# Performance work log

Measured on AMD Instinct MI355X. Metric: run time of the kernel, lower is better.

The kernel has to match this reference:

```python
import jax, jax.numpy as jnp
import numpy as np

B, N = 4096, 12
HID = 64
SLOPE = 0.2   # GATv2Conv default negative_slope
ALPHA = 0.1   # skip-connection scale


def _gabriel_adjacency(p):
    # p: [B, N, 2] node positions. Gabriel graph: edge (i,j) iff no other
    # point k lies inside the closed disk with diameter segment (p_i, p_j).
    n = p.shape[1]
    mid = (p[:, :, None, :] + p[:, None, :, :]) * 0.5                      # [B,N,N,2]
    r2 = jnp.sum((p[:, :, None, :] - p[:, None, :, :]) ** 2, -1) * 0.25    # [B,N,N]
    d2 = jnp.sum((p[:, None, None, :, :] - mid[:, :, :, None, :]) ** 2, -1)  # [B,i,j,k]
    eye = jnp.eye(n, dtype=bool)
    excl = eye[:, None, :] | eye[None, :, :]                               # k==i or k==j
    d2 = jnp.where(excl[None], jnp.inf, d2)
    gab = jnp.all(d2 > r2[..., None], axis=-1) & (~eye)[None]
    # undirected edges + self loops (GATv2Conv add_self_loops=True default)
    return gab | jnp.swapaxes(gab, 1, 2) | eye[None]                       # [B,N,N]


def _gatv2(x, adj, wl, wr, att, b):
    # PyG GATv2Conv, heads=1: e_ij = att . leaky_relu(W_l x_j + W_r x_i),
    # alpha = softmax_j(e_ij) over neighbors, out_i = sum_j alpha_ij W_l x_j + b.
    xl = x @ wl                                                            # source feats [B,N,H]
    xr = x @ wr                                                            # target feats [B,N,H]
    s = jax.nn.leaky_relu(xl[:, None, :, :] + xr[:, :, None, :], SLOPE)    # [B,i,j,H]
    e = jnp.einsum('bijh,h->bij', s, att)
    e = jnp.where(adj, e, -1e9)
    a = jax.nn.softmax(e, axis=-1)                                         # over sources j
    return jnp.einsum('bij,bjh->bih', a, xl) + b


def _forward(batch, enc_w1, enc_b1, enc_w2, enc_b2, enc_w3, enc_b3,
             g1_wl, g1_wr, g1_att, g1_b, g2_wl, g2_wr, g2_att, g2_b,
             g3_wl, g3_wr, g3_att, g3_b, g4_wl, g4_wr, g4_att, g4_b,
             lab_w, lab_b, val_w, val_b, skip_w, skip_b):
    h = jax.nn.relu(batch @ enc_w1 + enc_b1)
    h = jax.nn.relu(h @ enc_w2 + enc_b2)
    latent = h @ enc_w3 + enc_b3                                           # [B,N,3]
    # graph construction is non-differentiable (scipy in the original)
    adj = _gabriel_adjacency(jax.lax.stop_gradient(latent[..., :2]))
    x0 = latent[..., 2:3]                                                  # [B,N,1]
    x1 = jax.nn.relu(_gatv2(x0, adj, g1_wl, g1_wr, g1_att, g1_b))
    x2 = jax.nn.relu(_gatv2(x1, adj, g2_wl, g2_wr, g2_att, g2_b))
    skip = latent @ skip_w + skip_b
    x3 = jax.nn.relu(_gatv2(x2, adj, g3_wl, g3_wr, g3_att, g3_b) + ALPHA * skip)
    logits = x3 @ lab_w + lab_b                                            # [B,N,4]
    # note: original feeds x2 (not x3) into gcn4 -- kept faithful
    x4 = jax.nn.relu(_gatv2(x2, adj, g4_wl, g4_wr, g4_att, g4_b) + ALPHA * skip)
    values = x4 @ val_w + val_b                                            # [B,N,1]
    return batch[:, :, :4], batch[:, :, 4:5], logits, values, latent


def setup_inputs():
    key = jax.random.key(0)
    ks = iter(jax.random.split(key, 40))
    def rnd(shape, s=0.1):
        return jax.random.normal(next(ks), shape, dtype=jnp.float32) * s
    inp = {"batch": jax.random.normal(next(ks), (B, N, 5), dtype=jnp.float32)}
    inp.update(enc_w1=rnd((5, HID)), enc_b1=jnp.zeros((HID,), jnp.float32),
               enc_w2=rnd((HID, HID)), enc_b2=jnp.zeros((HID,), jnp.float32),
               enc_w3=rnd((HID, 3)), enc_b3=jnp.zeros((3,), jnp.float32))
    for i, cin in zip((1, 2, 3, 4), (1, HID, HID, HID)):
        inp[f"g{i}_wl"] = rnd((cin, HID)); inp[f"g{i}_wr"] = rnd((cin, HID))
        inp[f"g{i}_att"] = rnd((HID,)); inp[f"g{i}_b"] = jnp.zeros((HID,), jnp.float32)
    inp.update(lab_w=rnd((HID, 4)), lab_b=jnp.zeros((4,), jnp.float32),
               val_w=rnd((HID, 1)), val_b=jnp.zeros((1,), jnp.float32),
               skip_w=rnd((3, HID)), skip_b=jnp.zeros((HID,), jnp.float32))
    return inp


def reference(batch, enc_w1, enc_b1, enc_w2, enc_b2, enc_w3, enc_b3,
              g1_wl, g1_wr, g1_att, g1_b, g2_wl, g2_wr, g2_att, g2_b,
              g3_wl, g3_wr, g3_att, g3_b, g4_wl, g4_wr, g4_att, g4_b,
              lab_w, lab_b, val_w, val_b, skip_w, skip_b):
    return _forward(batch, enc_w1, enc_b1, enc_w2, enc_b2, enc_w3, enc_b3,
                    g1_wl, g1_wr, g1_att, g1_b, g2_wl, g2_wr, g2_att, g2_b,
                    g3_wl, g3_wr, g3_att, g3_b, g4_wl, g4_wr, g4_att, g4_b,
                    lab_w, lab_b, val_w, val_b, skip_w, skip_b)
```

## Files before the change

kernel.cpp:

```cpp
#include <hip/hip_runtime.h>
#include <hip/hip_bf16.h>
#include <math.h>

#define N     12
#define HID   64
#define STP   68
#define SLOPE 0.2f
#define ALPHA 0.1f

typedef float v2f __attribute__((ext_vector_type(2)));
typedef float v4f __attribute__((ext_vector_type(4)));
typedef int   i4  __attribute__((ext_vector_type(4)));
typedef short v8s __attribute__((ext_vector_type(8)));

static __device__ __forceinline__ v8s as_v8s(i4 v) {
    union { i4 a; v8s b; } u; u.a = v; return u.b;
}

#define OUT0 0
#define OUT1 196608
#define OUT2 245760
#define OUT3 442368
#define OUT4 491520

__global__ void prep_kernel(const float* __restrict__ enc_w2,
                            const float* __restrict__ g2_wl, const float* __restrict__ g2_wr,
                            const float* __restrict__ g3_wl, const float* __restrict__ g3_wr,
                            const float* __restrict__ g4_wl, const float* __restrict__ g4_wr,
                            const float* __restrict__ lab_w,
                            float* __restrict__ ws) {
    int t = threadIdx.x;
    int bx = blockIdx.x;
    if (bx < 64) {
        int c = bx;
        ws[t*64 + c] = enc_w2[c*64 + t];
        return;
    }
    if (bx == 112) {
        #pragma unroll
        for (int c = 0; c < 4; c++) ws[16384 + c*64 + t] = lab_w[t*4 + c];
        return;
    }
    int idx = bx - 64;
    int mat = idx >> 3, rem = idx & 7;
    int kt = rem >> 2, nt = rem & 3;
    const float* src;
    switch (mat) {
        case 0: src = g2_wl; break;
        case 1: src = g2_wr; break;
        case 2: src = g3_wl; break;
        case 3: src = g3_wr; break;
        case 4: src = g4_wl; break;
        default: src = g4_wr; break;
    }
    int quad = t >> 4, col = t & 15;
    int n = nt*16 + col;
    unsigned* dst = (unsigned*)(ws + 4096) + mat*2048 + (kt*4+nt)*256 + t*4;
    #pragma unroll
    for (int jp = 0; jp < 4; jp++) {
        int k0 = kt*32 + quad*8 + 2*jp;
        __hip_bfloat16 h0 = __float2bfloat16(src[(k0+0)*64 + n]);
        __hip_bfloat16 h1 = __float2bfloat16(src[(k0+1)*64 + n]);
        unsigned u0 = *(unsigned short*)&h0, u1 = *(unsigned short*)&h1;
        dst[jp] = u0 | (u1 << 16);
    }
}

template<bool TW>
__global__ __launch_bounds__(64, 3) void gae_kernel(
    const float* __restrict__ batch,
    const float* __restrict__ enc_w1, const float* __restrict__ enc_b1,
    const float* __restrict__ enc_w2, const float* __restrict__ enc_b2,
    const float* __restrict__ enc_w3, const float* __restrict__ enc_b3,
    const float* __restrict__ g1_wl, const float* __restrict__ g1_wr,
    const float* __restrict__ g1_att, const float* __restrict__ g1_b,
    const float* __restrict__ g2_wl, const float* __restrict__ g2_wr,
    const float* __restrict__ g2_att, const float* __restrict__ g2_b,
    const float* __restrict__ g3_wl, const float* __restrict__ g3_wr,
    const float* __restrict__ g3_att, const float* __restrict__ g3_b,
    const float* __restrict__ g4_wl, const float* __restrict__ g4_wr,
    const float* __restrict__ g4_att, const float* __restrict__ g4_b,
    const float* __restrict__ lab_w, const float* __restrict__ lab_b,
    const float* __restrict__ val_w, const float* __restrict__ val_b,
    const float* __restrict__ skip_w, const float* __restrict__ skip_b,
    const float* __restrict__ wsT,
    float* __restrict__ out)
{
    const int b = blockIdx.x;
    const int t = threadIdx.x;

    __shared__ __align__(16) float lds[2560];
    float* bufL = lds;
    float* bufR = lds + N*STP;
    float* xB   = lds + 2*N*STP;
    float* pool = lds + 2*N*STP + N*HID;
    unsigned char* pairs8 = (unsigned char*)&lds[2544];

    const v2f z2 = {0.f, 0.f};
    const v4f z4 = {0.f, 0.f, 0.f, 0.f};
    const v4f s4 = {SLOPE, SLOPE, SLOPE, SLOPE};

    const int p0 = t,        i0 = p0 / N, j0 = p0 - i0*N;
    const int p1 = t + 64,   i1 = p1 / N, j1 = p1 - i1*N;
    const int p2 = (t < 16) ? (t + 128) : 143;
    const int i2 = p2 / N,   j2 = p2 - i2*N;

    if (t < N*5) {
        float v = batch[b*(N*5) + t];
        pool[t] = v;
        int i = t / 5, f = t - i*5;
        if (f < 4) out[OUT0 + (size_t)b*(N*4) + i*4 + f] = v;
        else       out[OUT1 + (size_t)b*N + i] = v;
    }
    __syncthreads();

    {
        float acc[N];
        float bias = enc_b1[t];
        #pragma unroll
        for (int i=0;i<N;i++) acc[i] = bias;
        #pragma unroll
        for (int f=0; f<5; f++) {
            float w = enc_w1[f*HID + t];
            #pragma unroll
            for (int i=0;i<N;i++) acc[i] = fmaf(pool[i*5+f], w, acc[i]);
        }
        #pragma unroll
        for (int i=0;i<N;i++) bufL[i*STP + t] = fmaxf(acc[i], 0.f);
    }
    __syncthreads();

    {
        v2f acc[N];
        #pragma unroll
        for (int i=0;i<N;i++) acc[i] = z2;
        const float* w2p = TW ? (wsT + t*HID) : nullptr;
        for (int c=0;c<HID;c+=4) {
            v2f w01, w23;
            if (TW) {
                v4f w4 = *reinterpret_cast<const v4f*>(&w2p[c]);
                w01 = w4.xy; w23 = w4.zw;
            } else {
                w01 = (v2f){enc_w2[(c+0)*HID+t], enc_w2[(c+1)*HID+t]};
                w23 = (v2f){enc_w2[(c+2)*HID+t], enc_w2[(c+3)*HID+t]};
            }
            #pragma unroll
            for (int i=0;i<N;i++) {
                v4f xv = *reinterpret_cast<const v4f*>(&bufL[i*STP + c]);
                acc[i] = __builtin_elementwise_fma(xv.xy, w01, acc[i]);
                acc[i] = __builtin_elementwise_fma(xv.zw, w23, acc[i]);
            }
        }
        float bias = enc_b2[t];
        #pragma unroll
        for (int i=0;i<N;i++) bufR[i*STP + t] = fmaxf(bias + acc[i].x + acc[i].y, 0.f);
    }
    __syncthreads();

    if (t < N*3) {
        int i = t / 3, c = t - i*3;
        float acc = enc_b3[c];
        for (int k=0;k<HID;k+=4) {
            v4f xv = *reinterpret_cast<const v4f*>(&bufR[i*STP + k]);
            acc = fmaf(xv.x, enc_w3[(k+0)*3+c], acc);
            acc = fmaf(xv.y, enc_w3[(k+1)*3+c], acc);
            acc = fmaf(xv.z, enc_w3[(k+2)*3+c], acc);
            acc = fmaf(xv.w, enc_w3[(k+3)*3+c], acc);
        }
        pool[t] = acc;
        out[OUT4 + (size_t)b*(N*3) + t] = acc;
    }
    __syncthreads();

    float skipv[N];
    {
        float w0 = skip_w[t], w1 = skip_w[HID+t], w2 = skip_w[2*HID+t];
        float bias = skip_b[t];
        #pragma unroll
        for (int i=0;i<N;i++) {
            float v = bias;
            v = fmaf(pool[i*3+0], w0, v);
            v = fmaf(pool[i*3+1], w1, v);
            v = fmaf(pool[i*3+2], w2, v);
            skipv[i] = v;
        }
    }

    auto gab = [&](int i, int j)->bool {
        if (i == j) return false;
        float pix = pool[i*3], piy = pool[i*3+1];
        float pjx = pool[j*3], pjy = pool[j*3+1];
        float mx = (pix + pjx) * 0.5f, my = (piy + pjy) * 0.5f;
        float dx = pix - pjx, dy = piy - pjy;
        float r2 = (dx*dx + dy*dy) * 0.25f;
        bool g = true;
        #pragma unroll
        for (int k=0;k<N;k++) {
            float ex = pool[k*3] - mx, ey = pool[k*3+1] - my;
            bool ok = (k == i) || (k == j) || (ex*ex + ey*ey > r2);
            g = g && ok;
        }
        return g;
    };
    unsigned long long gb0 = __ballot(gab(i0, j0));
    unsigned long long gb1 = __ballot(gab(i1, j1));
    unsigned long long gb2 = __ballot((t < 16) && gab(i2, j2));
    auto gbit = [&](int p)->int {
        unsigned long long m = (p < 64) ? gb0 : ((p < 128) ? gb1 : gb2);
        return (int)((m >> (p & 63)) & 1ull);
    };
    const int adjA = gbit(p0) | gbit(j0*N+i0) | (i0 == j0);
    const int adjB = gbit(p1) | gbit(j1*N+i1) | (i1 == j1);
    const int adjC = (t < 16) ? (gbit(p2) | gbit(j2*N+i2) | (i2 == j2)) : 0;

    auto mbcnt64 = [&](unsigned long long m)->int {
        return __builtin_amdgcn_mbcnt_hi((unsigned)(m >> 32),
               __builtin_amdgcn_mbcnt_lo((unsigned)m, 0));
    };
    const unsigned long long am0 = __ballot(adjA != 0);
    const unsigned long long am1 = __ballot(adjB != 0);
    const unsigned long long am2 = __ballot(adjC != 0);
    const int c0  = __popcll(am0);
    const int c01 = c0 + __popcll(am1);
    const int nv  = c01 + __popcll(am2);
    const int idx0 = mbcnt64(am0);
    const int idx1 = c0  + mbcnt64(am1);
    const int idx2 = c01 + mbcnt64(am2);
    if (adjA)               pairs8[idx0] = (unsigned char)p0;
    if (adjB && idx1 < 64)  pairs8[idx1] = (unsigned char)p1;
    if (adjC && idx2 < 64)  pairs8[idx2] = (unsigned char)p2;
    const bool ovB = adjB && (idx1 >= 64);
    const bool ovC = adjC && (idx2 >= 64);
    const int nvc = nv < 64 ? nv : 64;

    auto scoreAt = [&](int i, int j, const float* __restrict__ att)->float {
        const float* Lj = &bufL[j*STP];
        const float* Ri = &bufR[i*STP];
        v4f a = z4;
        for (int h=0; h<HID; h+=4) {
            v4f a4 = *reinterpret_cast<const v4f*>(&att[h]);
            v4f xl = *reinterpret_cast<const v4f*>(Lj + h);
            v4f xr = *reinterpret_cast<const v4f*>(Ri + h);
            v4f s = xl + xr;
            v4f l = __builtin_elementwise_fma(s4, __builtin_elementwise_min(s, z4),
                                              __builtin_elementwise_max(s, z4));
            a = __builtin_elementwise_fma(a4, l, a);
        }
        return (a.x + a.y) + (a.z + a.w);
    };

    auto gat_core = [&](const float* __restrict__ att, const float* __restrict__ gb,
                        float* __restrict__ xout, int strideOut, int useSkip) {
        __syncthreads();
        pool[t] = -1e9f; pool[t+64] = -1e9f;
        if (t < 16) pool[t+128] = -1e9f;
        if (t < nvc) {
            int p = pairs8[t];
            int i = (p * 171) >> 11;
            int j = p - i*N;
            pool[p] = scoreAt(i, j, att);
        }
        if (nv > 64) {
            if (ovB) pool[p1] = scoreAt(i1, j1, att);
            if (ovC) pool[p2] = scoreAt(i2, j2, att);
        }
        __syncthreads();
        if (t < N) {
            float m = -2e9f;
            #pragma unroll
            for (int j=0;j<N;j++) m = fmaxf(m, pool[t*N+j]);
            float tmp[N]; float sum = 0.f;
            #pragma unroll
            for (int j=0;j<N;j++) { float v = __expf(pool[t*N+j] - m); tmp[j] = v; sum += v; }
            float inv = 1.0f / sum;
            #pragma unroll
            for (int j=0;j<N;j++) pool[t*N+j] = tmp[j] * inv;
        }
        __syncthreads();
        {
            float xj[N];
            #pragma unroll
            for (int j=0;j<N;j++) xj[j] = bufL[j*STP + t];
            v4f X0 = {xj[0], xj[1], xj[2],  xj[3]};
            v4f X1 = {xj[4], xj[5], xj[6],  xj[7]};
            v4f X2 = {xj[8], xj[9], xj[10], xj[11]};
            float bias = gb[t];
            #pragma unroll
            for (int i=0;i<N;i++) {
                const v4f* ep = reinterpret_cast<const v4f*>(&pool[i*N]);
                v4f acc = __builtin_elementwise_fma(ep[0], X0,
                          __builtin_elementwise_fma(ep[1], X1, ep[2]*X2));
                float r = bias + ((acc.x + acc.y) + (acc.z + acc.w));
                if (useSkip) r = fmaf(ALPHA, skipv[i], r);
                xout[i*strideOut + t] = fmaxf(r, 0.f);
            }
        }
        __syncthreads();
    };

    auto stage_mfma = [&](const float* __restrict__ xin, int strideIn, int matL) {
        const int m = t & 15, quad = t >> 4;
        const int mc = (m < N) ? m : 0;
        i4 aF[2];
        #pragma unroll
        for (int kt=0; kt<2; kt++) {
            const float* xp = &xin[mc*strideIn + kt*32 + quad*8];
            v4f lo = *reinterpret_cast<const v4f*>(xp);
            v4f hi = *reinterpret_cast<const v4f*>(xp + 4);
            unsigned u0 = __float_as_uint(lo.x) + 0x8000u, u1 = __float_as_uint(lo.y) + 0x8000u;
            unsigned u2 = __float_as_uint(lo.z) + 0x8000u, u3 = __float_as_uint(lo.w) + 0x8000u;
            unsigned u4 = __float_as_uint(hi.x) + 0x8000u, u5 = __float_as_uint(hi.y) + 0x8000u;
            unsigned u6 = __float_as_uint(hi.z) + 0x8000u, u7 = __float_as_uint(hi.w) + 0x8000u;
            i4 a;
            a.x = (int)__builtin_amdgcn_perm(u1, u0, 0x07060302u);
            a.y = (int)__builtin_amdgcn_perm(u3, u2, 0x07060302u);
            a.z = (int)__builtin_amdgcn_perm(u5, u4, 0x07060302u);
            a.w = (int)__builtin_amdgcn_perm(u7, u6, 0x07060302u);
            aF[kt] = a;
        }
        const i4* bbase = reinterpret_cast<const i4*>(wsT + 4096);
        #pragma unroll
        for (int mm=0; mm<2; mm++) {
            const i4* bp = bbase + (matL + mm)*512;
            v4f acc[4] = {z4, z4, z4, z4};
            #pragma unroll
            for (int nt=0; nt<4; nt++) {
                i4 b0 = bp[(0*4+nt)*64 + t];
                i4 b1 = bp[(1*4+nt)*64 + t];
                acc[nt] = __builtin_amdgcn_mfma_f32_16x16x32_bf16(as_v8s(aF[0]), as_v8s(b0), acc[nt], 0, 0, 0);
                acc[nt] = __builtin_amdgcn_mfma_f32_16x16x32_bf16(as_v8s(aF[1]), as_v8s(b1), acc[nt], 0, 0, 0);
            }
            float* dst = (mm == 0) ? bufL : bufR;
            if (quad < 3) {
                #pragma unroll
                for (int nt=0; nt<4; nt++) {
                    #pragma unroll
                    for (int r=0; r<4; r++)
                        dst[(quad*4+r)*STP + nt*16 + m] = acc[nt][r];
                }
            }
        }
    };

    auto stage = [&](const float* __restrict__ xin, int strideIn,
                     const float* __restrict__ wl, const float* __restrict__ wr) {
        v2f al[N], ar[N];
        #pragma unroll
        for (int i=0;i<N;i++) { al[i] = z2; ar[i] = z2; }
        for (int c=0;c<HID;c+=4) {
            v2f wl01 = (v2f){wl[(c+0)*HID+t], wl[(c+1)*HID+t]};
            v2f wl23 = (v2f){wl[(c+2)*HID+t], wl[(c+3)*HID+t]};
            v2f wr01 = (v2f){wr[(c+0)*HID+t], wr[(c+1)*HID+t]};
            v2f wr23 = (v2f){wr[(c+2)*HID+t], wr[(c+3)*HID+t]};
            #pragma unroll
            for (int i=0;i<N;i++) {
                v4f xv = *reinterpret_cast<const v4f*>(&xin[i*strideIn + c]);
                al[i] = __builtin_elementwise_fma(xv.xy, wl01, al[i]);
                al[i] = __builtin_elementwise_fma(xv.zw, wl23, al[i]);
                ar[i] = __builtin_elementwise_fma(xv.xy, wr01, ar[i]);
                ar[i] = __builtin_elementwise_fma(xv.zw, wr23, ar[i]);
            }
        }
        #pragma unroll
        for (int i=0;i<N;i++) {
            bufL[i*STP + t] = al[i].x + al[i].y;
            bufR[i*STP + t] = ar[i].x + ar[i].y;
        }
    };

    {
        float wlv = g1_wl[t], wrv = g1_wr[t];
        #pragma unroll
        for (int i=0;i<N;i++) {
            float v = pool[i*3+2];
            bufL[i*STP + t] = v * wlv;
            bufR[i*STP + t] = v * wrv;
        }
    }
    gat_core(g1_att, g1_b, bufR, STP, 0);

    if (TW) stage_mfma(bufR, STP, 0); else stage(bufR, STP, g2_wl, g2_wr);
    gat_core(g2_att, g2_b, xB, HID, 0);

    if (TW) stage_mfma(xB, HID, 2); else stage(xB, HID, g3_wl, g3_wr);
    gat_core(g3_att, g3_b, bufR, STP, 1);

    if (t < N*4) {
        int i = t >> 2, c = t & 3;
        float acc = lab_b[c];
        if (TW) {
            const float* lwT = wsT + 16384 + c*HID;
            for (int h=0;h<HID;h+=4) {
                v4f xv = *reinterpret_cast<const v4f*>(&bufR[i*STP + h]);
                v4f w4 = *reinterpret_cast<const v4f*>(&lwT[h]);
                acc = fmaf(xv.x, w4.x, acc);
                acc = fmaf(xv.y, w4.y, acc);
                acc = fmaf(xv.z, w4.z, acc);
                acc = fmaf(xv.w, w4.w, acc);
            }
        } else {
            for (int h=0;h<HID;h+=4) {
                v4f xv = *reinterpret_cast<const v4f*>(&bufR[i*STP + h]);
                acc = fmaf(xv.x, lab_w[(h+0)*4+c], acc);
                acc = fmaf(xv.y, lab_w[(h+1)*4+c], acc);
                acc = fmaf(xv.z, lab_w[(h+2)*4+c], acc);
                acc = fmaf(xv.w, lab_w[(h+3)*4+c], acc);
            }
        }
        out[OUT2 + (size_t)b*(N*4) + t] = acc;
    }

    if (TW) stage_mfma(xB, HID, 4); else stage(xB, HID, g4_wl, g4_wr);
    gat_core(g4_att, g4_b, bufR, STP, 1);

    if (t < N) {
        float acc = val_b[0];
        for (int h=0;h<HID;h+=4) {
            v4f xv = *reinterpret_cast<const v4f*>(&bufR[t*STP + h]);
            v4f w4 = *reinterpret_cast<const v4f*>(&val_w[h]);
            acc = fmaf(xv.x, w4.x, acc);
            acc = fmaf(xv.y, w4.y, acc);
            acc = fmaf(xv.z, w4.z, acc);
            acc = fmaf(xv.w, w4.w, acc);
        }
        out[OUT3 + (size_t)b*N + t] = acc;
    }
}

extern "C" void kernel_launch(void* const* d_in, const int* in_sizes, int n_in,
                              void* d_out, int out_size, void* d_ws, size_t ws_size,
                              hipStream_t stream) {
    (void)in_sizes; (void)n_in; (void)out_size;
    const bool useT = (ws_size >= (16384 + 256)*sizeof(float));
    if (useT) {
        prep_kernel<<<dim3(113), dim3(64), 0, stream>>>(
            (const float*)d_in[3],
            (const float*)d_in[11], (const float*)d_in[12],
            (const float*)d_in[15], (const float*)d_in[16],
            (const float*)d_in[19], (const float*)d_in[20],
            (const float*)d_in[23],
            (float*)d_ws);
        gae_kernel<true><<<dim3(4096), dim3(64), 0, stream>>>(
            (const float*)d_in[0],
            (const float*)d_in[1],  (const float*)d_in[2],
            (const float*)d_in[3],  (const float*)d_in[4],
            (const float*)d_in[5],  (const float*)d_in[6],
            (const float*)d_in[7],  (const float*)d_in[8],  (const float*)d_in[9],  (const float*)d_in[10],
            (const float*)d_in[11], (const float*)d_in[12], (const float*)d_in[13], (const float*)d_in[14],
            (const float*)d_in[15], (const float*)d_in[16], (const float*)d_in[17], (const float*)d_in[18],
            (const float*)d_in[19], (const float*)d_in[20], (const float*)d_in[21], (const float*)d_in[22],
            (const float*)d_in[23], (const float*)d_in[24],
            (const float*)d_in[25], (const float*)d_in[26],
            (const float*)d_in[27], (const float*)d_in[28],
            (const float*)d_ws,
            (float*)d_out);
    } else {
        gae_kernel<false><<<dim3(4096), dim3(64), 0, stream>>>(
            (const float*)d_in[0],
            (const float*)d_in[1],  (const float*)d_in[2],
            (const float*)d_in[3],  (const float*)d_in[4],
            (const float*)d_in[5],  (const float*)d_in[6],
            (const float*)d_in[7],  (const float*)d_in[8],  (const float*)d_in[9],  (const float*)d_in[10],
            (const float*)d_in[11], (const float*)d_in[12], (const float*)d_in[13], (const float*)d_in[14],
            (const float*)d_in[15], (const float*)d_in[16], (const float*)d_in[17], (const float*)d_in[18],
            (const float*)d_in[19], (const float*)d_in[20], (const float*)d_in[21], (const float*)d_in[22],
            (const float*)d_in[23], (const float*)d_in[24],
            (const float*)d_in[25], (const float*)d_in[26],
            (const float*)d_in[27], (const float*)d_in[28],
            nullptr,
            (float*)d_out);
    }
}
```

Before: 155.1 us.

## Split each graph across two wavefronts with row-partitioned work and per-wave MFMA matrices

Launches 128 threads per graph instead of 64. Each wavefront owns six of the twelve node rows for the encoder, softmax and aggregation, and the two waves split the left and right projection matrices in the MFMA stage. Score computation is halved across lane groups and recombined with shuffles, and the Gabriel adjacency ballots are exchanged through LDS. The aim is more parallel work per graph and lower per-thread register pressure, enabling higher occupancy. The cost is extra barriers and cross-wave LDS traffic.

New measurement: 207.4 us. 33.7% more time.

```diff
diff --git a/kernel.cpp b/kernel.cpp
--- a/kernel.cpp
+++ b/kernel.cpp
@@ -67,7 +67,7 @@
 }
 
 template<bool TW>
-__global__ __launch_bounds__(64, 3) void gae_kernel(
+__global__ __launch_bounds__(128, 8) void gae_kernel(
     const float* __restrict__ batch,
     const float* __restrict__ enc_w1, const float* __restrict__ enc_b1,
     const float* __restrict__ enc_w2, const float* __restrict__ enc_b2,
@@ -88,218 +88,283 @@
 {
     const int b = blockIdx.x;
     const int t = threadIdx.x;
-
-    __shared__ __align__(16) float lds[2560];
-    float* bufL = lds;
-    float* bufR = lds + N*STP;
-    float* xB   = lds + 2*N*STP;
-    float* pool = lds + 2*N*STP + N*HID;
-    unsigned char* pairs8 = (unsigned char*)&lds[2544];
+    const int w = t >> 6;
+    const int l = t & 63;
+    const int r0 = w * 6;
+
+    __shared__ __align__(16) float lds[2544];
+    float* bufL  = lds;
+    float* bufR  = lds + N*STP;
+    float* xB    = lds + 2*N*STP;
+    float* pool  = lds + 2*N*STP + N*HID;
+    float* coord = pool + 108;
 
     const v2f z2 = {0.f, 0.f};
     const v4f z4 = {0.f, 0.f, 0.f, 0.f};
     const v4f s4 = {SLOPE, SLOPE, SLOPE, SLOPE};
 
-    const int p0 = t,        i0 = p0 / N, j0 = p0 - i0*N;
-    const int p1 = t + 64,   i1 = p1 / N, j1 = p1 - i1*N;
-    const int p2 = (t < 16) ? (t + 128) : 143;
-    const int i2 = p2 / N,   j2 = p2 - i2*N;
-
-    if (t < N*5) {
-        float v = batch[b*(N*5) + t];
-        pool[t] = v;
-        int i = t / 5, f = t - i*5;
+    if (l < 30) {
+        int idx = w*30 + l;
+        float v = batch[b*(N*5) + idx];
+        pool[idx] = v;
+        int i = idx / 5, f = idx - (idx/5)*5;
         if (f < 4) out[OUT0 + (size_t)b*(N*4) + i*4 + f] = v;
         else       out[OUT1 + (size_t)b*N + i] = v;
     }
-    __syncthreads();
 
     {
-        float acc[N];
-        float bias = enc_b1[t];
-        #pragma unroll
-        for (int i=0;i<N;i++) acc[i] = bias;
+        float acc[6];
+        float bias = enc_b1[l];
+        #pragma unroll
+        for (int i=0;i<6;i++) acc[i] = bias;
         #pragma unroll
         for (int f=0; f<5; f++) {
-            float w = enc_w1[f*HID + t];
-            #pragma unroll
-            for (int i=0;i<N;i++) acc[i] = fmaf(pool[i*5+f], w, acc[i]);
-        }
-        #pragma unroll
-        for (int i=0;i<N;i++) bufL[i*STP + t] = fmaxf(acc[i], 0.f);
-    }
-    __syncthreads();
+            float wv = enc_w1[f*HID + l];
+            #pragma unroll
+            for (int i=0;i<6;i++) acc[i] = fmaf(pool[(r0+i)*5+f], wv, acc[i]);
+        }
+        #pragma unroll
+        for (int i=0;i<6;i++) bufL[(r0+i)*STP + l] = fmaxf(acc[i], 0.f);
+    }
 
     {
-        v2f acc[N];
-        #pragma unroll
-        for (int i=0;i<N;i++) acc[i] = z2;
-        const float* w2p = TW ? (wsT + t*HID) : nullptr;
+        v2f acc[6];
+        #pragma unroll
+        for (int i=0;i<6;i++) acc[i] = z2;
+        const float* w2p = TW ? (wsT + l*HID) : nullptr;
         for (int c=0;c<HID;c+=4) {
             v2f w01, w23;
             if (TW) {
                 v4f w4 = *reinterpret_cast<const v4f*>(&w2p[c]);
                 w01 = w4.xy; w23 = w4.zw;
             } else {
-                w01 = (v2f){enc_w2[(c+0)*HID+t], enc_w2[(c+1)*HID+t]};
-                w23 = (v2f){enc_w2[(c+2)*HID+t], enc_w2[(c+3)*HID+t]};
-            }
-            #pragma unroll
-            for (int i=0;i<N;i++) {
-                v4f xv = *reinterpret_cast<const v4f*>(&bufL[i*STP + c]);
+                w01 = (v2f){enc_w2[(c+0)*HID+l], enc_w2[(c+1)*HID+l]};
+                w23 = (v2f){enc_w2[(c+2)*HID+l], enc_w2[(c+3)*HID+l]};
+            }
+            #pragma unroll
+            for (int i=0;i<6;i++) {
+                v4f xv = *reinterpret_cast<const v4f*>(&bufL[(r0+i)*STP + c]);
                 acc[i] = __builtin_elementwise_fma(xv.xy, w01, acc[i]);
                 acc[i] = __builtin_elementwise_fma(xv.zw, w23, acc[i]);
             }
         }
-        float bias = enc_b2[t];
-        #pragma unroll
-        for (int i=0;i<N;i++) bufR[i*STP + t] = fmaxf(bias + acc[i].x + acc[i].y, 0.f);
-    }
-    __syncthreads();
-
-    if (t < N*3) {
-        int i = t / 3, c = t - i*3;
-        float acc = enc_b3[c];
-        for (int k=0;k<HID;k+=4) {
+        float bias = enc_b2[l];
+        #pragma unroll
+        for (int i=0;i<6;i++) bufR[(r0+i)*STP + l] = fmaxf(bias + acc[i].x + acc[i].y, 0.f);
+    }
+
+    if (l < 36) {
+        int i   = r0 + l/6;
+        int rem = l - (l/6)*6;
+        int c   = rem >> 1, sb = rem & 1;
+        float acc = 0.f;
+        for (int k = sb*32; k < sb*32 + 32; k += 4) {
             v4f xv = *reinterpret_cast<const v4f*>(&bufR[i*STP + k]);
             acc = fmaf(xv.x, enc_w3[(k+0)*3+c], acc);
             acc = fmaf(xv.y, enc_w3[(k+1)*3+c], acc);
             acc = fmaf(xv.z, enc_w3[(k+2)*3+c], acc);
             acc = fmaf(xv.w, enc_w3[(k+3)*3+c], acc);
         }
-        pool[t] = acc;
-        out[OUT4 + (size_t)b*(N*3) + t] = acc;
+        acc += __shfl_xor(acc, 1);
+        if (sb == 0) {
+            acc += enc_b3[c];
+            coord[i*3 + c] = acc;
+            out[OUT4 + (size_t)b*(N*3) + i*3 + c] = acc;
+        }
+    }
+
+    float skipv[6];
+    {
+        float w0 = skip_w[l], w1 = skip_w[HID+l], w2v = skip_w[2*HID+l];
+        float bias = skip_b[l];
+        #pragma unroll
+        for (int i=0;i<6;i++) {
+            float v = bias;
+            v = fmaf(coord[(r0+i)*3+0], w0, v);
+            v = fmaf(coord[(r0+i)*3+1], w1, v);
+            v = fmaf(coord[(r0+i)*3+2], w2v, v);
+            skipv[i] = v;
+        }
     }
     __syncthreads();
-
-    float skipv[N];
-    {
-        float w0 = skip_w[t], w1 = skip_w[HID+t], w2 = skip_w[2*HID+t];
-        float bias = skip_b[t];
-        #pragma unroll
-        for (int i=0;i<N;i++) {
-            float v = bias;
-            v = fmaf(pool[i*3+0], w0, v);
-            v = fmaf(pool[i*3+1], w1, v);
-            v = fmaf(pool[i*3+2], w2, v);
-            skipv[i] = v;
-        }
-    }
 
     auto gab = [&](int i, int j)->bool {
         if (i == j) return false;
-        float pix = pool[i*3], piy = pool[i*3+1];
-        float pjx = pool[j*3], pjy = pool[j*3+1];
+        float pix = coord[i*3], piy = coord[i*3+1];
+        float pjx = coord[j*3], pjy = coord[j*3+1];
         float mx = (pix + pjx) * 0.5f, my = (piy + pjy) * 0.5f;
         float dx = pix - pjx, dy = piy - pjy;
         float r2 = (dx*dx + dy*dy) * 0.25f;
         bool g = true;
         #pragma unroll
         for (int k=0;k<N;k++) {
-            float ex = pool[k*3] - mx, ey = pool[k*3+1] - my;
+            float ex = coord[k*3] - mx, ey = coord[k*3+1] - my;
             bool ok = (k == i) || (k == j) || (ex*ex + ey*ey > r2);
             g = g && ok;
         }
         return g;
     };
-    unsigned long long gb0 = __ballot(gab(i0, j0));
-    unsigned long long gb1 = __ballot(gab(i1, j1));
-    unsigned long long gb2 = __ballot((t < 16) && gab(i2, j2));
+    unsigned* pu = (unsigned*)(pool + 64);
+    if (w == 0) {
+        int i0 = (l*171) >> 11, j0 = l - i0*N;
+        unsigned long long m0 = __ballot(gab(i0, j0));
+        if (l == 0) { pu[0] = (unsigned)m0; pu[1] = (unsigned)(m0 >> 32); }
+    } else {
+        int p1 = 64 + l;
+        int i1 = (p1*171) >> 11, j1 = p1 - i1*N;
+        unsigned long long m1 = __ballot(gab(i1, j1));
+        int p2 = (l < 16) ? (128 + l) : 143;
+        int i2 = (p2*171) >> 11, j2 = p2 - i2*N;
+        unsigned long long m2 = __ballot((l < 16) && gab(i2, j2));
+        if (l == 0) { pu[2] = (unsigned)m1; pu[3] = (unsigned)(m1 >> 32);
+                      pu[4] = (unsigned)m2; pu[5] = (unsigned)(m2 >> 32); }
+    }
+    __syncthreads();
+
+    const unsigned long long gb0 = (unsigned long long)pu[0] | ((unsigned long long)pu[1] << 32);
+    const unsigned long long gb1 = (unsigned long long)pu[2] | ((unsigned long long)pu[3] << 32);
+    const unsigned long long gb2 = (unsigned long long)pu[4] | ((unsigned long long)pu[5] << 32);
     auto gbit = [&](int p)->int {
         unsigned long long m = (p < 64) ? gb0 : ((p < 128) ? gb1 : gb2);
         return (int)((m >> (p & 63)) & 1ull);
     };
-    const int adjA = gbit(p0) | gbit(j0*N+i0) | (i0 == j0);
-    const int adjB = gbit(p1) | gbit(j1*N+i1) | (i1 == j1);
-    const int adjC = (t < 16) ? (gbit(p2) | gbit(j2*N+i2) | (i2 == j2)) : 0;
-
     auto mbcnt64 = [&](unsigned long long m)->int {
         return __builtin_amdgcn_mbcnt_hi((unsigned)(m >> 32),
                __builtin_amdgcn_mbcnt_lo((unsigned)m, 0));
     };
-    const unsigned long long am0 = __ballot(adjA != 0);
-    const unsigned long long am1 = __ballot(adjB != 0);
-    const unsigned long long am2 = __ballot(adjC != 0);
-    const int c0  = __popcll(am0);
-    const int c01 = c0 + __popcll(am1);
-    const int nv  = c01 + __popcll(am2);
-    const int idx0 = mbcnt64(am0);
-    const int idx1 = c0  + mbcnt64(am1);
-    const int idx2 = c01 + mbcnt64(am2);
-    if (adjA)               pairs8[idx0] = (unsigned char)p0;
-    if (adjB && idx1 < 64)  pairs8[idx1] = (unsigned char)p1;
-    if (adjC && idx2 < 64)  pairs8[idx2] = (unsigned char)p2;
-    const bool ovB = adjB && (idx1 >= 64);
-    const bool ovC = adjC && (idx2 >= 64);
-    const int nvc = nv < 64 ? nv : 64;
-
-    auto scoreAt = [&](int i, int j, const float* __restrict__ att)->float {
+
+    unsigned rowm = 0;
+    if (l < 12) {
+        int ri = r0 + (l >> 1);
+        #pragma unroll
+        for (int j=0;j<N;j++)
+            rowm |= (unsigned)(gbit(ri*N + j) | gbit(j*N + ri) | (ri == j)) << j;
+    }
+
+    int nW = 0;
+    bool ovC = false; int im2 = 0, jm2 = 0, myp2 = 0;
+    unsigned char* mylist = (unsigned char*)(pool + 72) + w*64;
+    if (w == 0) {
+        int i0 = (l*171) >> 11, j0 = l - i0*N;
+        int a = gbit(l) | gbit(j0*N + i0) | (i0 == j0);
+        unsigned long long am = __ballot(a != 0);
+        if (a) mylist[mbcnt64(am)] = (unsigned char)l;
+        nW = __popcll(am);
+    } else {
+        int p1 = 64 + l;
+        int i1 = (p1*171) >> 11, j1 = p1 - i1*N;
+        int aB = gbit(p1) | gbit(j1*N + i1) | (i1 == j1);
+        int p2 = (l < 16) ? (128 + l) : 143;
+        int i2 = (p2*171) >> 11, j2 = p2 - i2*N;
+        int aC = (l < 16) ? (gbit(p2) | gbit(j2*N + i2) | (i2 == j2)) : 0;
+        unsigned long long am1 = __ballot(aB != 0);
+        unsigned long long am2 = __ballot(aC != 0);
+        int c1 = __popcll(am1);
+        int idx1 = mbcnt64(am1);
+        int idx2 = c1 + mbcnt64(am2);
+        if (aB) mylist[idx1] = (unsigned char)p1;
+        if (aC && idx2 < 64) mylist[idx2] = (unsigned char)p2;
+        ovC = aC && (idx2 >= 64);
+        im2 = i2; jm2 = j2; myp2 = p2;
+        int n = c1 + __popcll(am2);
+        nW = n < 64 ? n : 64;
+    }
+    const int pidm = l & 31, sub = l >> 5;
+    const bool actA = pidm < nW;
+    const bool actB = (32 + pidm) < nW;
+    const bool anyB = nW > 32;
+    int pA = 0, iA = 0, jA = 0, pB = 0, iB = 0, jB = 0;
+    if (actA) { pA = mylist[pidm];      iA = (pA*171) >> 11; jA = pA - iA*N; }
+    if (actB) { pB = mylist[32 + pidm]; iB = (pB*171) >> 11; jB = pB - iB*N; }
+
+    auto scoreHalf = [&](int i, int j, const float* __restrict__ att)->float {
+        const float* Lj = &bufL[j*STP + sub*32];
+        const float* Ri = &bufR[i*STP + sub*32];
+        const float* ah = att + sub*32;
+        v4f a = z4;
+        for (int h=0; h<32; h+=4) {
+            v4f a4 = *reinterpret_cast<const v4f*>(&ah[h]);
+            v4f xl = *reinterpret_cast<const v4f*>(&Lj[h]);
+            v4f xr = *reinterpret_cast<const v4f*>(&Ri[h]);
+            v4f s = xl + xr;
+            v4f lr = __builtin_elementwise_fma(s4, __builtin_elementwise_min(s, z4),
+                                               __builtin_elementwise_max(s, z4));
+            a = __builtin_elementwise_fma(a4, lr, a);
+        }
+        return (a.x + a.y) + (a.z + a.w);
+    };
+    auto scoreFull = [&](int i, int j, const float* __restrict__ att)->float {
         const float* Lj = &bufL[j*STP];
         const float* Ri = &bufR[i*STP];
         v4f a = z4;
         for (int h=0; h<HID; h+=4) {
             v4f a4 = *reinterpret_cast<const v4f*>(&att[h]);
-            v4f xl = *reinterpret_cast<const v4f*>(Lj + h);
-            v4f xr = *reinterpret_cast<const v4f*>(Ri + h);
+            v4f xl = *reinterpret_cast<const v4f*>(&Lj[h]);
+            v4f xr = *reinterpret_cast<const v4f*>(&Ri[h]);
             v4f s = xl + xr;
-            v4f l = __builtin_elementwise_fma(s4, __builtin_elementwise_min(s, z4),
-                                              __builtin_elementwise_max(s, z4));
-            a = __builtin_elementwise_fma(a4, l, a);
+            v4f lr = __builtin_elementwise_fma(s4, __builtin_elementwise_min(s, z4),
+                                               __builtin_elementwise_max(s, z4));
+            a = __builtin_elementwise_fma(a4, lr, a);
         }
         return (a.x + a.y) + (a.z + a.w);
     };
 
-    auto gat_core = [&](const float* __restrict__ att, const float* __restrict__ gb,
+    auto gat_core = [&](const float* __restrict__ att, const float* __restrict__ gbias,
                         float* __restrict__ xout, int strideOut, int useSkip) {
         __syncthreads();
-        pool[t] = -1e9f; pool[t+64] = -1e9f;
-        if (t < 16) pool[t+128] = -1e9f;
-        if (t < nvc) {
-            int p = pairs8[t];
-            int i = (p * 171) >> 11;
-            int j = p - i*N;
-            pool[p] = scoreAt(i, j, att);
-        }
-        if (nv > 64) {
-            if (ovB) pool[p1] = scoreAt(i1, j1, att);
-            if (ovC) pool[p2] = scoreAt(i2, j2, att);
+        {
+            float sA = scoreHalf(iA, jA, att);
+            sA += __shfl_xor(sA, 32);
+            if (actA && sub == 0) pool[pA] = sA;
+            if (anyB) {
+                float sB = scoreHalf(iB, jB, att);
+                sB += __shfl_xor(sB, 32);
+                if (actB && sub == 0) pool[pB] = sB;
+            }
+            if (w == 1 && ovC) pool[myp2] = scoreFull(im2, jm2, att);
         }
         __syncthreads();
-        if (t < N) {
-            float m = -2e9f;
-            #pragma unroll
-            for (int j=0;j<N;j++) m = fmaxf(m, pool[t*N+j]);
-            float tmp[N]; float sum = 0.f;
-            #pragma unroll
-            for (int j=0;j<N;j++) { float v = __expf(pool[t*N+j] - m); tmp[j] = v; sum += v; }
+        if (l < 12) {
+            int i  = r0 + (l >> 1);
+            int j0 = (l & 1) * 6;
+            float ev[6]; float m = -2e9f;
+            #pragma unroll
+            for (int jj=0; jj<6; jj++) {
+                float v = ((rowm >> (j0 + jj)) & 1u) ? pool[i*N + j0 + jj] : -1e9f;
+                ev[jj] = v; m = fmaxf(m, v);
+            }
+            m = fmaxf(m, __shfl_xor(m, 1));
+            float sum = 0.f;
+            #pragma unroll
+            for (int jj=0; jj<6; jj++) { float e = __expf(ev[jj] - m); ev[jj] = e; sum += e; }
+            sum += __shfl_xor(sum, 1);
             float inv = 1.0f / sum;
             #pragma unroll
-            for (int j=0;j<N;j++) pool[t*N+j] = tmp[j] * inv;
-        }
-        __syncthreads();
+            for (int jj=0; jj<6; jj++) pool[i*N + j0 + jj] = ev[jj] * inv;
+        }
         {
             float xj[N];
             #pragma unroll
-            for (int j=0;j<N;j++) xj[j] = bufL[j*STP + t];
+            for (int j=0;j<N;j++) xj[j] = bufL[j*STP + l];
             v4f X0 = {xj[0], xj[1], xj[2],  xj[3]};
             v4f X1 = {xj[4], xj[5], xj[6],  xj[7]};
             v4f X2 = {xj[8], xj[9], xj[10], xj[11]};
-            float bias = gb[t];
-            #pragma unroll
-            for (int i=0;i<N;i++) {
-                const v4f* ep = reinterpret_cast<const v4f*>(&pool[i*N]);
+            float bias = gbias[l];
+            #pragma unroll
+            for (int i=0;i<6;i++) {
+                const v4f* ep = reinterpret_cast<const v4f*>(&pool[(r0+i)*N]);
                 v4f acc = __builtin_elementwise_fma(ep[0], X0,
                           __builtin_elementwise_fma(ep[1], X1, ep[2]*X2));
                 float r = bias + ((acc.x + acc.y) + (acc.z + acc.w));
                 if (useSkip) r = fmaf(ALPHA, skipv[i], r);
-                xout[i*strideOut + t] = fmaxf(r, 0.f);
-            }
-        }
+                xout[(r0+i)*strideOut + l] = fmaxf(r, 0.f);
+            }
+        }
+    };
+
+    auto stage_mfma = [&](const float* __restrict__ xin, int strideIn, int matBase) {
         __syncthreads();
-    };
-
-    auto stage_mfma = [&](const float* __restrict__ xin, int strideIn, int matL) {
-        const int m = t & 15, quad = t >> 4;
+        const int m = l & 15, quad = l >> 4;
         const int mc = (m < N) ? m : 0;
         i4 aF[2];
         #pragma unroll
@@ -318,80 +383,78 @@
             a.w = (int)__builtin_amdgcn_perm(u7, u6, 0x07060302u);
             aF[kt] = a;
         }
-        const i4* bbase = reinterpret_cast<const i4*>(wsT + 4096);
-        #pragma unroll
-        for (int mm=0; mm<2; mm++) {
-            const i4* bp = bbase + (matL + mm)*512;
-            v4f acc[4] = {z4, z4, z4, z4};
+        const i4* bp = reinterpret_cast<const i4*>(wsT + 4096) + (matBase + w)*512;
+        v4f acc[4] = {z4, z4, z4, z4};
+        #pragma unroll
+        for (int nt=0; nt<4; nt++) {
+            i4 b0 = bp[nt*64 + l];
+            i4 b1 = bp[(4+nt)*64 + l];
+            acc[nt] = __builtin_amdgcn_mfma_f32_16x16x32_bf16(as_v8s(aF[0]), as_v8s(b0), acc[nt], 0, 0, 0);
+            acc[nt] = __builtin_amdgcn_mfma_f32_16x16x32_bf16(as_v8s(aF[1]), as_v8s(b1), acc[nt], 0, 0, 0);
+        }
+        float* dst = w ? bufR : bufL;
+        if (quad < 3) {
             #pragma unroll
             for (int nt=0; nt<4; nt++) {
-                i4 b0 = bp[(0*4+nt)*64 + t];
-                i4 b1 = bp[(1*4+nt)*64 + t];
-                acc[nt] = __builtin_amdgcn_mfma_f32_16x16x32_bf16(as_v8s(aF[0]), as_v8s(b0), acc[nt], 0, 0, 0);
-                acc[nt] = __builtin_amdgcn_mfma_f32_16x16x32_bf16(as_v8s(aF[1]), as_v8s(b1), acc[nt], 0, 0, 0);
-            }
-            float* dst = (mm == 0) ? bufL : bufR;
-            if (quad < 3) {
                 #pragma unroll
-                for (int nt=0; nt<4; nt++) {
-                    #pragma unroll
-                    for (int r=0; r<4; r++)
-                        dst[(quad*4+r)*STP + nt*16 + m] = acc[nt][r];
+                for (int r=0; r<4; r++)
+                    dst[(quad*4+r)*STP + nt*16 + m] = acc[nt][r];
+            }
+        }
+    };
+
+    auto stage_f32 = [&](const float* __restrict__ xin, int strideIn,
+                         const float* __restrict__ wl, const float* __restrict__ wr) {
+        __syncthreads();
+        const float* wm = w ? wr : wl;
+        float* dst = w ? bufR : bufL;
+        #pragma unroll
+        for (int half=0; half<2; half++) {
+            v2f acc[6];
+            #pragma unroll
+            for (int i=0;i<6;i++) acc[i] = z2;
+            for (int c=0;c<HID;c+=4) {
+                v2f w01 = (v2f){wm[(c+0)*HID+l], wm[(c+1)*HID+l]};
+                v2f w23 = (v2f){wm[(c+2)*HID+l], wm[(c+3)*HID+l]};
+                #pragma unroll
+                for (int i=0;i<6;i++) {
+                    v4f xv = *reinterpret_cast<const v4f*>(&xin[(half*6+i)*strideIn + c]);
+                    acc[i] = __builtin_elementwise_fma(xv.xy, w01, acc[i]);
+                    acc[i] = __builtin_elementwise_fma(xv.zw, w23, acc[i]);
                 }
             }
-        }
-    };
-
-    auto stage = [&](const float* __restrict__ xin, int strideIn,
-                     const float* __restrict__ wl, const float* __restrict__ wr) {
-        v2f al[N], ar[N];
-        #pragma unroll
-        for (int i=0;i<N;i++) { al[i] = z2; ar[i] = z2; }
-        for (int c=0;c<HID;c+=4) {
-            v2f wl01 = (v2f){wl[(c+0)*HID+t], wl[(c+1)*HID+t]};
-            v2f wl23 = (v2f){wl[(c+2)*HID+t], wl[(c+3)*HID+t]};
-            v2f wr01 = (v2f){wr[(c+0)*HID+t], wr[(c+1)*HID+t]};
-            v2f wr23 = (v2f){wr[(c+2)*HID+t], wr[(c+3)*HID+t]};
-            #pragma unroll
-            for (int i=0;i<N;i++) {
-                v4f xv = *reinterpret_cast<const v4f*>(&xin[i*strideIn + c]);
-                al[i] = __builtin_elementwise_fma(xv.xy, wl01, al[i]);
-                al[i] = __builtin_elementwise_fma(xv.zw, wl23, al[i]);
-                ar[i] = __builtin_elementwise_fma(xv.xy, wr01, ar[i]);
-                ar[i] = __builtin_elementwise_fma(xv.zw, wr23, ar[i]);
-            }
-        }
-        #pragma unroll
-        for (int i=0;i<N;i++) {
-            bufL[i*STP + t] = al[i].x + al[i].y;
-            bufR[i*STP + t] = ar[i].x + ar[i].y;
+            #pragma unroll
+            for (int i=0;i<6;i++) dst[(half*6+i)*STP + l] = acc[i].x + acc[i].y;
         }
     };
 
     {
-        float wlv = g1_wl[t], wrv = g1_wr[t];
-        #pragma unroll
-        for (int i=0;i<N;i++) {
-            float v = pool[i*3+2];
-            bufL[i*STP + t] = v * wlv;
-            bufR[i*STP + t] = v * wrv;
-        }
-    }
-    gat_core(g1_att, g1_b, bufR, STP, 0);
-
-    if (TW) stage_mfma(bufR, STP, 0); else stage(bufR, STP, g2_wl, g2_wr);
+        float wlv = g1_wl[l], wrv = g1_wr[l];
+        #pragma unroll
+        for (int i=0;i<6;i++) {
+            float v = coord[(r0+i)*3 + 2];
+            bufL[(r0+i)*STP + l] = v * wlv;
+            bufR[(r0+i)*STP + l] = v * wrv;
+        }
+    }
+    gat_core(g1_att, g1_b, xB, HID, 0);
+
+    if (TW) stage_mfma(xB, HID, 0); else stage_f32(xB, HID, g2_wl, g2_wr);
     gat_core(g2_att, g2_b, xB, HID, 0);
 
-    if (TW) stage_mfma(xB, HID, 2); else stage(xB, HID, g3_wl, g3_wr);
+    if (TW) stage_mfma(xB, HID, 2); else stage_f32(xB, HID, g3_wl, g3_wr);
     gat_core(g3_att, g3_b, bufR, STP, 1);
 
-    if (t < N*4) {
-        int i = t >> 2, c = t & 3;
-        float acc = lab_b[c];
+    if (l < 48) {
+        int i   = r0 + (l >> 3);
+        int rem = l & 7;
+        int c = rem >> 1, sb = rem & 1;
+        float acc = 0.f;
         if (TW) {
-            const float* lwT = wsT + 16384 + c*HID;
-            for (int h=0;h<HID;h+=4) {
-                v4f xv = *reinterpret_cast<const v4f*>(&bufR[i*STP + h]);
+            const float* lwT = wsT + 16384 + c*HID + sb*32;
+            const float* xr  = &bufR[i*STP + sb*32];
+            for (int h=0; h<32; h+=4) {
+                v4f xv = *reinterpret_cast<const v4f*>(&xr[h]);
                 v4f w4 = *reinterpret_cast<const v4f*>(&lwT[h]);
                 acc = fmaf(xv.x, w4.x, acc);
                 acc = fmaf(xv.y, w4.y, acc);
@@ -399,7 +462,7 @@
                 acc = fmaf(xv.w, w4.w, acc);
             }
         } else {
-            for (int h=0;h<HID;h+=4) {
+            for (int h = sb*32; h < sb*32 + 32; h += 4) {
                 v4f xv = *reinterpret_cast<const v4f*>(&bufR[i*STP + h]);
                 acc = fmaf(xv.x, lab_w[(h+0)*4+c], acc);
                 acc = fmaf(xv.y, lab_w[(h+1)*4+c], acc);
@@ -407,23 +470,29 @@
                 acc = fmaf(xv.w, lab_w[(h+3)*4+c], acc);
             }
         }
-        out[OUT2 + (size_t)b*(N*4) + t] = acc;
-    }
-
-    if (TW) stage_mfma(xB, HID, 4); else stage(xB, HID, g4_wl, g4_wr);
+        acc += __shfl_xor(acc, 1);
+        if (sb == 0) out[OUT2 + (size_t)b*(N*4) + i*4 + c] = acc + lab_b[c];
+    }
+
+    if (TW) stage_mfma(xB, HID, 4); else stage_f32(xB, HID, g4_wl, g4_wr);
     gat_core(g4_att, g4_b, bufR, STP, 1);
 
-    if (t < N) {
-        float acc = val_b[0];
-        for (int h=0;h<HID;h+=4) {
-            v4f xv = *reinterpret_cast<const v4f*>(&bufR[t*STP + h]);
-            v4f w4 = *reinterpret_cast<const v4f*>(&val_w[h]);
+    if (l < 12) {
+        int i  = r0 + (l >> 1);
+        int sb = l & 1;
+        float acc = 0.f;
+        const float* xr = &bufR[i*STP + sb*32];
+        const float* wv = val_w + sb*32;
+        for (int h=0; h<32; h+=4) {
+            v4f xv = *reinterpret_cast<const v4f*>(&xr[h]);
+            v4f w4 = *reinterpret_cast<const v4f*>(&wv[h]);
             acc = fmaf(xv.x, w4.x, acc);
             acc = fmaf(xv.y, w4.y, acc);
             acc = fmaf(xv.z, w4.z, acc);
             acc = fmaf(xv.w, w4.w, acc);
         }
-        out[OUT3 + (size_t)b*N + t] = acc;
+        acc += __shfl_xor(acc, 1);
+        if (sb == 0) out[OUT3 + (size_t)b*N + i] = acc + val_b[0];
     }
 }
 
@@ -440,7 +509,7 @@
             (const float*)d_in[19], (const float*)d_in[20],
             (const float*)d_in[23],
             (float*)d_ws);
-        gae_kernel<true><<<dim3(4096), dim3(64), 0, stream>>>(
+        gae_kernel<true><<<dim3(4096), dim3(128), 0, stream>>>(
             (const float*)d_in[0],
             (const float*)d_in[1],  (const float*)d_in[2],
             (const float*)d_in[3],  (const float*)d_in[4],
@@ -455,7 +524,7 @@
             (const float*)d_ws,
             (float*)d_out);
     } else {
-        gae_kernel<false><<<dim3(4096), dim3(64), 0, stream>>>(
+        gae_kernel<false><<<dim3(4096), dim3(128), 0, stream>>>(
             (const float*)d_in[0],
             (const float*)d_in[1],  (const float*)d_in[2],
             (const float*)d_in[3],  (const float*)d_in[4],
```
